# Performance work log

Hardware: AMD Instinct MI355X
Metric: run time of the kernel (lower is better)

The kernel has to match this reference:

```python
import jax, jax.numpy as jnp
import numpy as np

N_NODES = 100000

def setup_inputs() -> dict:
    key = jax.random.key(0)
    k1, k2, k3, k4, k5 = jax.random.split(key, 5)
    n_edges = 3200000
    row = jax.random.randint(k1, (n_edges,), 0, N_NODES)
    col = jax.random.randint(k2, (n_edges,), 0, N_NODES)
    vals = jax.random.uniform(k3, (n_edges,), dtype=jnp.float32)
    x = jax.random.normal(k4, (N_NODES, 128), dtype=jnp.float32)
    weight = jax.random.normal(k5, (128, 128), dtype=jnp.float32) * 0.05
    return {"row": row, "col": col, "vals": vals, "x": x, "weight": weight}

def reference(row, col, vals, x, weight):
    # SpMM: z[r] += vals[e] * x[col[e]]  (COO aggregation, equiv. to spmm_gpu over all blocks)
    gathered = vals[:, None] * x[col]                       # [E, F] gather + scale
    z = jax.ops.segment_sum(gathered, row, num_segments=N_NODES)  # [N, F] scatter-add
    return z @ weight                                        # dense GEMM [N, F] x [F, O]
```

## Files before the change

### kernel.cpp

```cpp
#include <hip/hip_runtime.h>
#include <hip/hip_bf16.h>

#define FDIM 128
#define BROWS 256
#define NBMAX 512
#define BCAP 9216
#define LDA 136

typedef __attribute__((ext_vector_type(8))) short short8v;
typedef __attribute__((ext_vector_type(4))) float f32x4;
typedef __attribute__((ext_vector_type(4))) unsigned uint4v;

__device__ __forceinline__ short f2bf(float f) {
    unsigned u = __float_as_uint(f);
    u += 0x7FFFu + ((u >> 16) & 1u);
    return (short)(u >> 16);
}

__global__ __launch_bounds__(256)
void gemm_mfma(const float* __restrict__ x, const float* __restrict__ W,
               unsigned short* __restrict__ y, int nrows) {
    __shared__ short ldsA[32 * LDA];
    const int lane = threadIdx.x & 63;
    const int wid  = threadIdx.x >> 6;
    const int colHalf = wid & 1;
    const int rowSub  = wid >> 1;
    const int l15 = lane & 15;
    const int lhi = lane >> 4;

    short8v bfrag[4][4];
    #pragma unroll
    for (int ks = 0; ks < 4; ++ks)
      #pragma unroll
      for (int ct = 0; ct < 4; ++ct) {
        const int col = colHalf * 64 + ct * 16 + l15;
        const int kb  = ks * 32 + lhi * 8;
        short8v f;
        #pragma unroll
        for (int j = 0; j < 8; ++j) f[j] = f2bf(W[(kb + j) * FDIM + col]);
        bfrag[ks][ct] = f;
      }

    const int lr  = threadIdx.x >> 3;
    const int lc  = (threadIdx.x & 7) * 16;

    const int nTiles = (nrows + 31) >> 5;
    for (int tile = blockIdx.x; tile < nTiles; tile += gridDim.x) {
        const int rowBase = tile * 32 + rowSub * 16;
        {
            int srow = tile * 32 + lr;
            if (srow >= nrows) srow = nrows - 1;
            const float* xp = x + (size_t)srow * FDIM + lc;
            float4 a = *(const float4*)(xp + 0);
            float4 b = *(const float4*)(xp + 4);
            float4 c = *(const float4*)(xp + 8);
            float4 d = *(const float4*)(xp + 12);
            short8v s0, s1;
            s0[0]=f2bf(a.x); s0[1]=f2bf(a.y); s0[2]=f2bf(a.z); s0[3]=f2bf(a.w);
            s0[4]=f2bf(b.x); s0[5]=f2bf(b.y); s0[6]=f2bf(b.z); s0[7]=f2bf(b.w);
            s1[0]=f2bf(c.x); s1[1]=f2bf(c.y); s1[2]=f2bf(c.z); s1[3]=f2bf(c.w);
            s1[4]=f2bf(d.x); s1[5]=f2bf(d.y); s1[6]=f2bf(d.z); s1[7]=f2bf(d.w);
            *(short8v*)&ldsA[lr * LDA + lc]     = s0;
            *(short8v*)&ldsA[lr * LDA + lc + 8] = s1;
        }
        __syncthreads();

        f32x4 acc[4] = {};
        #pragma unroll
        for (int ks = 0; ks < 4; ++ks) {
            short8v af = *(const short8v*)&ldsA[(rowSub * 16 + l15) * LDA + ks * 32 + lhi * 8];
            #pragma unroll
            for (int ct = 0; ct < 4; ++ct)
                acc[ct] = __builtin_amdgcn_mfma_f32_16x16x32_bf16(af, bfrag[ks][ct], acc[ct], 0, 0, 0);
        }
        #pragma unroll
        for (int ct = 0; ct < 4; ++ct) {
            const int col = colHalf * 64 + ct * 16 + l15;
            #pragma unroll
            for (int r = 0; r < 4; ++r) {
                int orow = rowBase + lhi * 4 + r;
                if (orow < nrows) y[(size_t)orow * FDIM + col] = (unsigned short)f2bf(acc[ct][r]);
            }
        }
        __syncthreads();
    }
}

__global__ __launch_bounds__(256)
void scatter_alloc(const int* __restrict__ row, const int* __restrict__ col,
                   const float* __restrict__ vals, int* __restrict__ gcur,
                   int2* __restrict__ skv1, int E, int per, int NB) {
    __shared__ int lc[NBMAX];
    __shared__ int cur[NBMAX];
    const int blk = blockIdx.x;
    for (int i = threadIdx.x; i < NB; i += 256) lc[i] = 0;
    __syncthreads();
    const int lo = blk * per;
    const int hi = (lo + per < E) ? lo + per : E;
    for (int i = lo + threadIdx.x; i < hi; i += 256)
        atomicAdd(&lc[row[i] >> 8], 1);
    __syncthreads();
    for (int i = threadIdx.x; i < NB; i += 256) {
        int c = lc[i];
        int base = c ? atomicAdd(&gcur[i], c) : 0;
        cur[i] = i * BCAP + base;
    }
    __syncthreads();
    for (int i = lo + threadIdx.x; i < hi; i += 256) {
        int r = row[i];
        int b = r >> 8;
        int pos = atomicAdd(&cur[b], 1);
        if (pos < (b + 1) * BCAP)
            skv1[pos] = make_int2(col[i] | ((r & 255) << 17), __float_as_int(vals[i]));
    }
}

__global__ __launch_bounds__(1024)
void sort_inplace(int2* __restrict__ skv1, const int* __restrict__ gcur,
                  int2* __restrict__ offs, int NB, int N) {
    __shared__ int2 ekv[BCAP];
    __shared__ int cnt[BROWS];
    __shared__ int cur[BROWS];
    __shared__ int ws4[4];
    const int tid = threadIdx.x;
    const int b   = blockIdx.x;
    const int start = b * BCAP;
    int total = gcur[b];
    if (total > BCAP) total = BCAP;

    if (tid < BROWS) cnt[tid] = 0;
    __syncthreads();
    for (int j = tid; j < total; j += 1024) {
        int2 kv = skv1[start + j];
        ekv[j] = kv;
        atomicAdd(&cnt[((unsigned)kv.x >> 17) & 255], 1);
    }
    __syncthreads();

    int c = 0, s = 0;
    if (tid < BROWS) {
        c = cnt[tid];
        s = c;
        const int lane = tid & 63;
        #pragma unroll
        for (int off = 1; off < 64; off <<= 1) {
            int t = __shfl_up(s, off, 64);
            if (lane >= off) s += t;
        }
        if (lane == 63) ws4[tid >> 6] = s;
    }
    __syncthreads();
    if (tid == 0) {
        int a0 = ws4[0], a1 = ws4[1], a2 = ws4[2];
        ws4[0] = 0; ws4[1] = a0; ws4[2] = a0 + a1; ws4[3] = a0 + a1 + a2;
    }
    __syncthreads();
    if (tid < BROWS) {
        int excl = s - c + ws4[tid >> 6];
        cur[tid] = excl;
        int gr = b * BROWS + tid;
        if (gr < N) offs[gr] = make_int2(start + excl, start + excl + c);
    }
    __syncthreads();

    for (int j = tid; j < total; j += 1024) {
        int2 kv = ekv[j];
        int rl = ((unsigned)kv.x >> 17) & 255;
        int pos = atomicAdd(&cur[rl], 1);
        skv1[start + pos] = make_int2(kv.x & 0x1FFFF, kv.y);
    }
}

__global__ __launch_bounds__(256)
void spmm_csr_v3(const int2* __restrict__ offs, const int2* __restrict__ skv,
                 const unsigned* __restrict__ yu, float* __restrict__ out, int N) {
    const int wid  = (blockIdx.x * 256 + threadIdx.x) >> 6;
    const int lane = threadIdx.x & 63;
    if (wid >= N) return;
    const int l15 = lane & 15;
    const int grp = lane >> 4;
    const int2 st = offs[wid];
    const int s = st.x, t = st.y;

    float accA[8] = {0,0,0,0,0,0,0,0};
    float accB[8] = {0,0,0,0,0,0,0,0};

    int e = s;
    for (; e + 8 <= t; e += 8) {
        int2 kA = skv[e + grp];
        int2 kB = skv[e + 4 + grp];
        uint4v uA = *(const uint4v*)&yu[(size_t)kA.x * 64 + l15 * 4];
        uint4v uB = *(const uint4v*)&yu[(size_t)kB.x * 64 + l15 * 4];
        float vA = __int_as_float(kA.y);
        float vB = __int_as_float(kB.y);
        #pragma unroll
        for (int j = 0; j < 4; ++j) {
            accA[2*j]   = fmaf(vA, __uint_as_float(uA[j] << 16),          accA[2*j]);
            accA[2*j+1] = fmaf(vA, __uint_as_float(uA[j] & 0xffff0000u), accA[2*j+1]);
            accB[2*j]   = fmaf(vB, __uint_as_float(uB[j] << 16),          accB[2*j]);
            accB[2*j+1] = fmaf(vB, __uint_as_float(uB[j] & 0xffff0000u), accB[2*j+1]);
        }
    }
    for (; e < t; e += 4) {
        int eA = e + grp;
        bool ok = eA < t;
        int2 kA = ok ? skv[eA] : make_int2(0, 0);
        uint4v uA = *(const uint4v*)&yu[(size_t)kA.x * 64 + l15 * 4];
        float vA = ok ? __int_as_float(kA.y) : 0.f;
        #pragma unroll
        for (int j = 0; j < 4; ++j) {
            accA[2*j]   = fmaf(vA, __uint_as_float(uA[j] << 16),          accA[2*j]);
            accA[2*j+1] = fmaf(vA, __uint_as_float(uA[j] & 0xffff0000u), accA[2*j+1]);
        }
    }
    #pragma unroll
    for (int j = 0; j < 8; ++j) {
        float a = accA[j] + accB[j];
        a += __shfl_xor(a, 16, 64);
        a += __shfl_xor(a, 32, 64);
        accA[j] = a;
    }
    if (grp == 0) {
        float* po = out + (size_t)wid * FDIM + l15 * 8;
        *(float4*)po       = make_float4(accA[0], accA[1], accA[2], accA[3]);
        *(float4*)(po + 4) = make_float4(accA[4], accA[5], accA[6], accA[7]);
    }
}

__global__ __launch_bounds__(256)
void edge_histogram(const int* __restrict__ row, int* __restrict__ counts, int E) {
    int i = blockIdx.x * 256 + threadIdx.x;
    if (i < E) atomicAdd(&counts[row[i]], 1);
}

__global__ __launch_bounds__(1024)
void scan_counts_v3(const int* __restrict__ counts, int* __restrict__ offsets,
                    int* __restrict__ cursor, int n, int ncopies, int stride) {
    const int tid  = threadIdx.x;
    const int lane = tid & 63;
    const int wv   = tid >> 6;
    __shared__ int waveSum[16];
    int carry = 0;
    const int nTiles = (n + 4095) >> 12;
    for (int tile = 0; tile < nTiles; ++tile) {
        const int idx = tile * 4096 + tid * 4;
        int4 v = make_int4(0, 0, 0, 0);
        if (idx + 3 < n) {
            for (int k = 0; k < ncopies; ++k) {
                int4 t = *(const int4*)&counts[(size_t)k * stride + idx];
                v.x += t.x; v.y += t.y; v.z += t.z; v.w += t.w;
            }
        } else if (idx < n) {
            for (int k = 0; k < ncopies; ++k) {
                const int* c = counts + (size_t)k * stride;
                v.x += c[idx];
                if (idx + 1 < n) v.y += c[idx + 1];
                if (idx + 2 < n) v.z += c[idx + 2];
            }
        }
        int s4 = v.x + v.y + v.z + v.w;
        int s = s4;
        #pragma unroll
        for (int off = 1; off < 64; off <<= 1) {
            int t = __shfl_up(s, off, 64);
            if (lane >= off) s += t;
        }
        if (lane == 63) waveSum[wv] = s;
        __syncthreads();
        if (tid < 64) {
            int ws = (tid < 16) ? waveSum[tid] : 0;
            #pragma unroll
            for (int off = 1; off < 16; off <<= 1) {
                int t = __shfl_up(ws, off, 64);
                if (lane >= off) ws += t;
            }
            if (tid < 16) waveSum[tid] = ws;
        }
        __syncthreads();
        const int waveBase = (wv == 0) ? 0 : waveSum[wv - 1];
        const int tileTot  = waveSum[15];
        int incl = s + waveBase + carry;
        int e0 = incl - s4;
        int4 o = make_int4(e0, e0 + v.x, e0 + v.x + v.y, e0 + v.x + v.y + v.z);
        if (idx + 3 < n) {
            *(int4*)&offsets[idx] = o;
            *(int4*)&cursor[idx]  = o;
        } else if (idx < n) {
            offsets[idx] = o.x;  cursor[idx] = o.x;
            if (idx + 1 < n) { offsets[idx + 1] = o.y; cursor[idx + 1] = o.y; }
            if (idx + 2 < n) { offsets[idx + 2] = o.z; cursor[idx + 2] = o.z; }
        }
        carry += tileTot;
        __syncthreads();
    }
    if (tid == 0) offsets[n] = carry;
}

__global__ __launch_bounds__(256)
void edge_scatter_chunked(const int* __restrict__ row, const int* __restrict__ col,
                          const float* __restrict__ vals, int* __restrict__ cursor,
                          int2* __restrict__ skv, int E, int rowsPerChunk) {
    const int chunk = blockIdx.x & 7;
    const int sub   = blockIdx.x >> 3;
    const int nsub  = gridDim.x >> 3;
    const int lo = chunk * rowsPerChunk;
    const int hi = lo + rowsPerChunk;
    for (int i = sub * 256 + threadIdx.x; i < E; i += nsub * 256) {
        int r = row[i];
        if (r >= lo && r < hi) {
            int pos = atomicAdd(&cursor[r], 1);
            skv[pos] = make_int2(col[i], __float_as_int(vals[i]));
        }
    }
}

__global__ __launch_bounds__(256)
void spmm_csr_v2(const int* __restrict__ offsets, const int2* __restrict__ skv,
                 const unsigned* __restrict__ yu, float* __restrict__ out, int N) {
    const int wid  = (blockIdx.x * 256 + threadIdx.x) >> 6;
    const int lane = threadIdx.x & 63;
    if (wid >= N) return;
    const int l15 = lane & 15;
    const int grp = lane >> 4;
    const int s = offsets[wid], t = offsets[wid + 1];

    float accA[8] = {0,0,0,0,0,0,0,0};
    float accB[8] = {0,0,0,0,0,0,0,0};

    int e = s;
    for (; e + 8 <= t; e += 8) {
        int2 kA = skv[e + grp];
        int2 kB = skv[e + 4 + grp];
        uint4v uA = *(const uint4v*)&yu[(size_t)kA.x * 64 + l15 * 4];
        uint4v uB = *(const uint4v*)&yu[(size_t)kB.x * 64 + l15 * 4];
        float vA = __int_as_float(kA.y);
        float vB = __int_as_float(kB.y);
        #pragma unroll
        for (int j = 0; j < 4; ++j) {
            accA[2*j]   = fmaf(vA, __uint_as_float(uA[j] << 16),          accA[2*j]);
            accA[2*j+1] = fmaf(vA, __uint_as_float(uA[j] & 0xffff0000u), accA[2*j+1]);
            accB[2*j]   = fmaf(vB, __uint_as_float(uB[j] << 16),          accB[2*j]);
            accB[2*j+1] = fmaf(vB, __uint_as_float(uB[j] & 0xffff0000u), accB[2*j+1]);
        }
    }
    for (; e < t; e += 4) {
        int eA = e + grp;
        bool ok = eA < t;
        int2 kA = ok ? skv[eA] : make_int2(0, 0);
        uint4v uA = *(const uint4v*)&yu[(size_t)kA.x * 64 + l15 * 4];
        float vA = ok ? __int_as_float(kA.y) : 0.f;
        #pragma unroll
        for (int j = 0; j < 4; ++j) {
            accA[2*j]   = fmaf(vA, __uint_as_float(uA[j] << 16),          accA[2*j]);
            accA[2*j+1] = fmaf(vA, __uint_as_float(uA[j] & 0xffff0000u), accA[2*j+1]);
        }
    }
    #pragma unroll
    for (int j = 0; j < 8; ++j) {
        float a = accA[j] + accB[j];
        a += __shfl_xor(a, 16, 64);
        a += __shfl_xor(a, 32, 64);
        accA[j] = a;
    }
    if (grp == 0) {
        float* po = out + (size_t)wid * FDIM + l15 * 8;
        *(float4*)po       = make_float4(accA[0], accA[1], accA[2], accA[3]);
        *(float4*)(po + 4) = make_float4(accA[4], accA[5], accA[6], accA[7]);
    }
}

__global__ __launch_bounds__(256)
void gemm_rows(const float* src, const float* __restrict__ W, float* dst, int nrows) {
    __shared__ float sW[FDIM * FDIM];
    for (int i = threadIdx.x; i < FDIM * FDIM; i += 256) sW[i] = W[i];
    __syncthreads();
    const int lane = threadIdx.x & 63;
    const int wid  = (blockIdx.x * 256 + threadIdx.x) >> 6;
    const int nw   = (gridDim.x * 256) >> 6;
    for (int n = wid; n < nrows; n += nw) {
        const float* xr = src + (size_t)n * FDIM;
        float acc0 = 0.f, acc1 = 0.f;
        #pragma unroll 8
        for (int k = 0; k < FDIM; ++k) {
            float xv = xr[k];
            float2 w = *(const float2*)&sW[k * FDIM + lane * 2];
            acc0 = fmaf(xv, w.x, acc0);
            acc1 = fmaf(xv, w.y, acc1);
        }
        *(float2*)&dst[(size_t)n * FDIM + lane * 2] = make_float2(acc0, acc1);
    }
}

__global__ __launch_bounds__(256)
void spmm_scatter(const int* __restrict__ row, const int* __restrict__ col,
                  const float* __restrict__ vals, const float* __restrict__ y,
                  float* __restrict__ out, int E) {
    long long tid = (long long)blockIdx.x * 256 + threadIdx.x;
    int e = (int)(tid >> 5);
    if (e >= E) return;
    int c = ((int)tid & 31) << 2;
    int r  = row[e];
    int cl = col[e];
    float v = vals[e];
    float4 yv = *(const float4*)&y[(size_t)cl * FDIM + c];
    float* po = out + (size_t)r * FDIM + c;
    unsafeAtomicAdd(po + 0, v * yv.x);
    unsafeAtomicAdd(po + 1, v * yv.y);
    unsafeAtomicAdd(po + 2, v * yv.z);
    unsafeAtomicAdd(po + 3, v * yv.w);
}

extern "C" void kernel_launch(void* const* d_in, const int* in_sizes, int n_in,
                              void* d_out, int out_size, void* d_ws, size_t ws_size,
                              hipStream_t stream) {
    const int*   row  = (const int*)d_in[0];
    const int*   col  = (const int*)d_in[1];
    const float* vals = (const float*)d_in[2];
    const float* x    = (const float*)d_in[3];
    const float* W    = (const float*)d_in[4];
    float* out = (float*)d_out;

    const int E = in_sizes[0];
    const int N = in_sizes[3] / FDIM;
    const int NB = (N + BROWS - 1) / BROWS;

    char* p = (char*)d_ws;
    unsigned short* yb = (unsigned short*)p;  p += (size_t)N * FDIM * 2;
    int*  gcur = (int*)p;   p += ((size_t)NB * 4 + 15) & ~(size_t)15;
    int2* offs = (int2*)p;  p += (size_t)N * 8;
    int2* skv1 = (int2*)p;  p += (size_t)NB * BCAP * 8;
    const size_t needA = (size_t)(p - (char*)d_ws);

    char* q = (char*)d_ws;
    unsigned short* ybB = (unsigned short*)q;  q += (size_t)N * FDIM * 2;
    int*  countsB  = (int*)q;  q += (size_t)N * 4;
    int*  offsetsB = (int*)q;  q += (size_t)(N + 1) * 4 + 12;
    int*  cursorB  = (int*)q;  q += (size_t)N * 4;
    int2* skvB     = (int2*)q; q += (size_t)E * 8;
    const size_t needB = (size_t)(q - (char*)d_ws);

    const int eb = (E + 255) / 256;
    const int rowsPerChunk = (N + 7) / 8;

    if (ws_size >= needA && NB <= NBMAX) {
        const int Bs = 512;
        const int per = (E + Bs - 1) / Bs;
        hipMemsetAsync(gcur, 0, (size_t)NB * 4, stream);
        gemm_mfma<<<512, 256, 0, stream>>>(x, W, yb, N);
        scatter_alloc<<<Bs, 256, 0, stream>>>(row, col, vals, gcur, skv1, E, per, NB);
        sort_inplace<<<NB, 1024, 0, stream>>>(skv1, gcur, offs, NB, N);
        spmm_csr_v3<<<((size_t)N * 64 + 255) / 256, 256, 0, stream>>>(offs, skv1, (const unsigned*)yb, out, N);
    } else if (ws_size >= needB) {
        hipMemsetAsync(countsB, 0, (size_t)N * 4, stream);
        gemm_mfma<<<512, 256, 0, stream>>>(x, W, ybB, N);
        edge_histogram<<<eb, 256, 0, stream>>>(row, countsB, E);
        scan_counts_v3<<<1, 1024, 0, stream>>>(countsB, offsetsB, cursorB, N, 1, 0);
        edge_scatter_chunked<<<2048, 256, 0, stream>>>(row, col, vals, cursorB, skvB, E, rowsPerChunk);
        spmm_csr_v2<<<((size_t)N * 64 + 255) / 256, 256, 0, stream>>>(offsetsB, skvB, (const unsigned*)ybB, out, N);
    } else if (ws_size >= (size_t)N * FDIM * 4) {
        float* yw = (float*)d_ws;
        hipMemsetAsync(d_out, 0, (size_t)out_size * sizeof(float), stream);
        gemm_rows<<<1024, 256, 0, stream>>>(x, W, yw, N);
        spmm_scatter<<<(E + 7) / 8, 256, 0, stream>>>(row, col, vals, yw, out, E);
    } else {
        hipMemsetAsync(d_out, 0, (size_t)out_size * sizeof(float), stream);
        spmm_scatter<<<(E + 7) / 8, 256, 0, stream>>>(row, col, vals, x, out, E);
        gemm_rows<<<1024, 256, 0, stream>>>(out, W, out, N);
    }
}
```

Baseline: 201.0 us.

## Fuse bucket sort into SpMM kernel using LDS-resident sorted edge indices

Merges the in-place bucket sort and the CSR SpMM into one kernel. Each block sorts its bucket's edges in LDS through an index permutation and then aggregates its rows straight from LDS, so the sorted edges are never written back to global memory and re-read, and one kernel launch plus the offsets array go away. Buckets shrink from 256 to 128 rows with a smaller capacity so the LDS footprint (edges plus indices) stays bounded, which doubles the block count. The trade-off is fewer, heavier blocks with one row per wave at a time, which may give less latency hiding for the gathers than the separate SpMM kernel, and the smaller per-bucket capacity gives less headroom against overflow.

```diff
diff --git a/kernel.cpp b/kernel.cpp
--- a/kernel.cpp
+++ b/kernel.cpp
@@ -2,9 +2,9 @@
 #include <hip/hip_bf16.h>
 
 #define FDIM 128
-#define BROWS 256
-#define NBMAX 512
-#define BCAP 9216
+#define BROWS 128
+#define BCAP 4800
+#define NBMX 1024
 #define LDA 136
 
 typedef __attribute__((ext_vector_type(8))) short short8v;
@@ -90,15 +90,15 @@
 void scatter_alloc(const int* __restrict__ row, const int* __restrict__ col,
                    const float* __restrict__ vals, int* __restrict__ gcur,
                    int2* __restrict__ skv1, int E, int per, int NB) {
-    __shared__ int lc[NBMAX];
-    __shared__ int cur[NBMAX];
+    __shared__ int lc[NBMX];
+    __shared__ int cur[NBMX];
     const int blk = blockIdx.x;
     for (int i = threadIdx.x; i < NB; i += 256) lc[i] = 0;
     __syncthreads();
     const int lo = blk * per;
     const int hi = (lo + per < E) ? lo + per : E;
     for (int i = lo + threadIdx.x; i < hi; i += 256)
-        atomicAdd(&lc[row[i] >> 8], 1);
+        atomicAdd(&lc[row[i] >> 7], 1);
     __syncthreads();
     for (int i = threadIdx.x; i < NB; i += 256) {
         int c = lc[i];
@@ -108,32 +108,35 @@
     __syncthreads();
     for (int i = lo + threadIdx.x; i < hi; i += 256) {
         int r = row[i];
-        int b = r >> 8;
+        int b = r >> 7;
         int pos = atomicAdd(&cur[b], 1);
         if (pos < (b + 1) * BCAP)
-            skv1[pos] = make_int2(col[i] | ((r & 255) << 17), __float_as_int(vals[i]));
-    }
-}
-
-__global__ __launch_bounds__(1024)
-void sort_inplace(int2* __restrict__ skv1, const int* __restrict__ gcur,
-                  int2* __restrict__ offs, int NB, int N) {
+            skv1[pos] = make_int2(col[i] | ((r & 127) << 17), __float_as_int(vals[i]));
+    }
+}
+
+__global__ __launch_bounds__(512)
+void sort_spmm(const int2* __restrict__ skv1, const int* __restrict__ gcur,
+               const unsigned* __restrict__ yu, float* __restrict__ out,
+               int NB, int N) {
     __shared__ int2 ekv[BCAP];
+    __shared__ unsigned short sidx[BCAP];
     __shared__ int cnt[BROWS];
+    __shared__ int rstart[BROWS];
     __shared__ int cur[BROWS];
-    __shared__ int ws4[4];
+    __shared__ int ws2[2];
     const int tid = threadIdx.x;
     const int b   = blockIdx.x;
-    const int start = b * BCAP;
+    const int gbase = b * BCAP;
     int total = gcur[b];
     if (total > BCAP) total = BCAP;
 
     if (tid < BROWS) cnt[tid] = 0;
     __syncthreads();
-    for (int j = tid; j < total; j += 1024) {
-        int2 kv = skv1[start + j];
+    for (int j = tid; j < total; j += 512) {
+        int2 kv = skv1[gbase + j];
         ekv[j] = kv;
-        atomicAdd(&cnt[((unsigned)kv.x >> 17) & 255], 1);
+        atomicAdd(&cnt[((unsigned)kv.x >> 17) & 127], 1);
     }
     __syncthreads();
 
@@ -147,83 +150,74 @@
             int t = __shfl_up(s, off, 64);
             if (lane >= off) s += t;
         }
-        if (lane == 63) ws4[tid >> 6] = s;
-    }
-    __syncthreads();
-    if (tid == 0) {
-        int a0 = ws4[0], a1 = ws4[1], a2 = ws4[2];
-        ws4[0] = 0; ws4[1] = a0; ws4[2] = a0 + a1; ws4[3] = a0 + a1 + a2;
-    }
+        if (lane == 63) ws2[tid >> 6] = s;
+    }
+    __syncthreads();
+    if (tid == 0) { int a0 = ws2[0]; ws2[0] = 0; ws2[1] = a0; }
     __syncthreads();
     if (tid < BROWS) {
-        int excl = s - c + ws4[tid >> 6];
-        cur[tid] = excl;
-        int gr = b * BROWS + tid;
-        if (gr < N) offs[gr] = make_int2(start + excl, start + excl + c);
-    }
-    __syncthreads();
-
-    for (int j = tid; j < total; j += 1024) {
-        int2 kv = ekv[j];
-        int rl = ((unsigned)kv.x >> 17) & 255;
+        int excl = s - c + ws2[tid >> 6];
+        rstart[tid] = excl;
+        cur[tid]    = excl;
+    }
+    __syncthreads();
+    for (int j = tid; j < total; j += 512) {
+        int rl = ((unsigned)ekv[j].x >> 17) & 127;
         int pos = atomicAdd(&cur[rl], 1);
-        skv1[start + pos] = make_int2(kv.x & 0x1FFFF, kv.y);
-    }
-}
-
-__global__ __launch_bounds__(256)
-void spmm_csr_v3(const int2* __restrict__ offs, const int2* __restrict__ skv,
-                 const unsigned* __restrict__ yu, float* __restrict__ out, int N) {
-    const int wid  = (blockIdx.x * 256 + threadIdx.x) >> 6;
-    const int lane = threadIdx.x & 63;
-    if (wid >= N) return;
-    const int l15 = lane & 15;
-    const int grp = lane >> 4;
-    const int2 st = offs[wid];
-    const int s = st.x, t = st.y;
-
-    float accA[8] = {0,0,0,0,0,0,0,0};
-    float accB[8] = {0,0,0,0,0,0,0,0};
-
-    int e = s;
-    for (; e + 8 <= t; e += 8) {
-        int2 kA = skv[e + grp];
-        int2 kB = skv[e + 4 + grp];
-        uint4v uA = *(const uint4v*)&yu[(size_t)kA.x * 64 + l15 * 4];
-        uint4v uB = *(const uint4v*)&yu[(size_t)kB.x * 64 + l15 * 4];
-        float vA = __int_as_float(kA.y);
-        float vB = __int_as_float(kB.y);
-        #pragma unroll
-        for (int j = 0; j < 4; ++j) {
-            accA[2*j]   = fmaf(vA, __uint_as_float(uA[j] << 16),          accA[2*j]);
-            accA[2*j+1] = fmaf(vA, __uint_as_float(uA[j] & 0xffff0000u), accA[2*j+1]);
-            accB[2*j]   = fmaf(vB, __uint_as_float(uB[j] << 16),          accB[2*j]);
-            accB[2*j+1] = fmaf(vB, __uint_as_float(uB[j] & 0xffff0000u), accB[2*j+1]);
-        }
-    }
-    for (; e < t; e += 4) {
-        int eA = e + grp;
-        bool ok = eA < t;
-        int2 kA = ok ? skv[eA] : make_int2(0, 0);
-        uint4v uA = *(const uint4v*)&yu[(size_t)kA.x * 64 + l15 * 4];
-        float vA = ok ? __int_as_float(kA.y) : 0.f;
-        #pragma unroll
-        for (int j = 0; j < 4; ++j) {
-            accA[2*j]   = fmaf(vA, __uint_as_float(uA[j] << 16),          accA[2*j]);
-            accA[2*j+1] = fmaf(vA, __uint_as_float(uA[j] & 0xffff0000u), accA[2*j+1]);
-        }
-    }
-    #pragma unroll
-    for (int j = 0; j < 8; ++j) {
-        float a = accA[j] + accB[j];
-        a += __shfl_xor(a, 16, 64);
-        a += __shfl_xor(a, 32, 64);
-        accA[j] = a;
-    }
-    if (grp == 0) {
-        float* po = out + (size_t)wid * FDIM + l15 * 8;
-        *(float4*)po       = make_float4(accA[0], accA[1], accA[2], accA[3]);
-        *(float4*)(po + 4) = make_float4(accA[4], accA[5], accA[6], accA[7]);
+        sidx[pos] = (unsigned short)j;
+    }
+    __syncthreads();
+
+    const int lane = tid & 63;
+    const int wv   = tid >> 6;
+    const int l15  = lane & 15;
+    const int grp  = lane >> 4;
+    for (int rr = wv; rr < BROWS; rr += 8) {
+        const int s0 = rstart[rr];
+        const int t0 = s0 + cnt[rr];
+        float accA[8] = {0,0,0,0,0,0,0,0};
+        float accB[8] = {0,0,0,0,0,0,0,0};
+        int e = s0;
+        for (; e + 8 <= t0; e += 8) {
+            int2 kA = ekv[sidx[e + grp]];
+            int2 kB = ekv[sidx[e + 4 + grp]];
+            uint4v uA = *(const uint4v*)&yu[(size_t)((unsigned)kA.x & 0x1FFFFu) * 64 + l15 * 4];
+            uint4v uB = *(const uint4v*)&yu[(size_t)((unsigned)kB.x & 0x1FFFFu) * 64 + l15 * 4];
+            float vA = __int_as_float(kA.y);
+            float vB = __int_as_float(kB.y);
+            #pragma unroll
+            for (int j = 0; j < 4; ++j) {
+                accA[2*j]   = fmaf(vA, __uint_as_float(uA[j] << 16),          accA[2*j]);
+                accA[2*j+1] = fmaf(vA, __uint_as_float(uA[j] & 0xffff0000u), accA[2*j+1]);
+                accB[2*j]   = fmaf(vB, __uint_as_float(uB[j] << 16),          accB[2*j]);
+                accB[2*j+1] = fmaf(vB, __uint_as_float(uB[j] & 0xffff0000u), accB[2*j+1]);
+            }
+        }
+        for (; e < t0; e += 4) {
+            int eA = e + grp;
+            bool ok = eA < t0;
+            int2 kA = ekv[sidx[ok ? eA : e]];
+            uint4v uA = *(const uint4v*)&yu[(size_t)((unsigned)kA.x & 0x1FFFFu) * 64 + l15 * 4];
+            float vA = ok ? __int_as_float(kA.y) : 0.f;
+            #pragma unroll
+            for (int j = 0; j < 4; ++j) {
+                accA[2*j]   = fmaf(vA, __uint_as_float(uA[j] << 16),          accA[2*j]);
+                accA[2*j+1] = fmaf(vA, __uint_as_float(uA[j] & 0xffff0000u), accA[2*j+1]);
+            }
+        }
+        #pragma unroll
+        for (int j = 0; j < 8; ++j) {
+            float a = accA[j] + accB[j];
+            a += __shfl_xor(a, 16, 64);
+            a += __shfl_xor(a, 32, 64);
+            accA[j] = a;
+        }
+        const int orow = b * BROWS + rr;
+        if (grp == 0 && orow < N) {
+            float* po = out + (size_t)orow * FDIM + l15 * 8;
+            *(float4*)po       = make_float4(accA[0], accA[1], accA[2], accA[3]);
+            *(float4*)(po + 4) = make_float4(accA[4], accA[5], accA[6], accA[7]);
+        }
     }
 }
 
@@ -427,7 +421,6 @@
     char* p = (char*)d_ws;
     unsigned short* yb = (unsigned short*)p;  p += (size_t)N * FDIM * 2;
     int*  gcur = (int*)p;   p += ((size_t)NB * 4 + 15) & ~(size_t)15;
-    int2* offs = (int2*)p;  p += (size_t)N * 8;
     int2* skv1 = (int2*)p;  p += (size_t)NB * BCAP * 8;
     const size_t needA = (size_t)(p - (char*)d_ws);
 
@@ -442,14 +435,13 @@
     const int eb = (E + 255) / 256;
     const int rowsPerChunk = (N + 7) / 8;
 
-    if (ws_size >= needA && NB <= NBMAX) {
+    if (ws_size >= needA && NB <= NBMX) {
         const int Bs = 512;
         const int per = (E + Bs - 1) / Bs;
         hipMemsetAsync(gcur, 0, (size_t)NB * 4, stream);
         gemm_mfma<<<512, 256, 0, stream>>>(x, W, yb, N);
         scatter_alloc<<<Bs, 256, 0, stream>>>(row, col, vals, gcur, skv1, E, per, NB);
-        sort_inplace<<<NB, 1024, 0, stream>>>(skv1, gcur, offs, NB, N);
-        spmm_csr_v3<<<((size_t)N * 64 + 255) / 256, 256, 0, stream>>>(offs, skv1, (const unsigned*)yb, out, N);
+        sort_spmm<<<NB, 512, 0, stream>>>(skv1, gcur, (const unsigned*)yb, out, NB, N);
     } else if (ws_size >= needB) {
         hipMemsetAsync(countsB, 0, (size_t)N * 4, stream);
         gemm_mfma<<<512, 256, 0, stream>>>(x, W, ybB, N);
```

Result: slower. 222.3 us (+10.6%).

## Co-schedule GEMM and edge scatter in one launch; unroll SpMM to four edge streams

Applied to the files above, without the earlier changes.

Merges the bf16 MFMA GEMM and the bucketed edge scatter into a single kernel whose blocks are split by block index. The two independent stages can then run concurrently on the GPU, and one launch boundary goes away. The SpMM kernel now keeps four independent accumulators and processes 16 edges per iteration, giving more gathers in flight to hide memory latency. The cost is higher register pressure in the SpMM and mixed LDS and register needs in the fused kernel, which may lower occupancy.

```diff
diff --git a/kernel.cpp b/kernel.cpp
--- a/kernel.cpp
+++ b/kernel.cpp
@@ -18,8 +18,239 @@
 }
 
 __global__ __launch_bounds__(256)
-void gemm_mfma(const float* __restrict__ x, const float* __restrict__ W,
-               unsigned short* __restrict__ y, int nrows) {
+void gemm_scatter(const float* __restrict__ x, const float* __restrict__ W,
+                  unsigned short* __restrict__ y, int nrows,
+                  const int* __restrict__ row, const int* __restrict__ col,
+                  const float* __restrict__ vals, int* __restrict__ gcur,
+                  int2* __restrict__ skv1, int E, int per, int NB, int GB) {
+    if ((int)blockIdx.x < GB) {
+        __shared__ short ldsA[32 * LDA];
+        const int lane = threadIdx.x & 63;
+        const int wid  = threadIdx.x >> 6;
+        const int colHalf = wid & 1;
+        const int rowSub  = wid >> 1;
+        const int l15 = lane & 15;
+        const int lhi = lane >> 4;
+
+        short8v bfrag[4][4];
+        #pragma unroll
+        for (int ks = 0; ks < 4; ++ks)
+          #pragma unroll
+          for (int ct = 0; ct < 4; ++ct) {
+            const int c = colHalf * 64 + ct * 16 + l15;
+            const int kb = ks * 32 + lhi * 8;
+            short8v f;
+            #pragma unroll
+            for (int j = 0; j < 8; ++j) f[j] = f2bf(W[(kb + j) * FDIM + c]);
+            bfrag[ks][ct] = f;
+          }
+
+        const int lr = threadIdx.x >> 3;
+        const int lc = (threadIdx.x & 7) * 16;
+
+        const int nTiles = (nrows + 31) >> 5;
+        for (int tile = blockIdx.x; tile < nTiles; tile += GB) {
+            const int rowBase = tile * 32 + rowSub * 16;
+            {
+                int srow = tile * 32 + lr;
+                if (srow >= nrows) srow = nrows - 1;
+                const float* xp = x + (size_t)srow * FDIM + lc;
+                float4 a = *(const float4*)(xp + 0);
+                float4 b = *(const float4*)(xp + 4);
+                float4 c = *(const float4*)(xp + 8);
+                float4 d = *(const float4*)(xp + 12);
+                short8v s0, s1;
+                s0[0]=f2bf(a.x); s0[1]=f2bf(a.y); s0[2]=f2bf(a.z); s0[3]=f2bf(a.w);
+                s0[4]=f2bf(b.x); s0[5]=f2bf(b.y); s0[6]=f2bf(b.z); s0[7]=f2bf(b.w);
+                s1[0]=f2bf(c.x); s1[1]=f2bf(c.y); s1[2]=f2bf(c.z); s1[3]=f2bf(c.w);
+                s1[4]=f2bf(d.x); s1[5]=f2bf(d.y); s1[6]=f2bf(d.z); s1[7]=f2bf(d.w);
+                *(short8v*)&ldsA[lr * LDA + lc]     = s0;
+                *(short8v*)&ldsA[lr * LDA + lc + 8] = s1;
+            }
+            __syncthreads();
+
+            f32x4 acc[4] = {};
+            #pragma unroll
+            for (int ks = 0; ks < 4; ++ks) {
+                short8v af = *(const short8v*)&ldsA[(rowSub * 16 + l15) * LDA + ks * 32 + lhi * 8];
+                #pragma unroll
+                for (int ct = 0; ct < 4; ++ct)
+                    acc[ct] = __builtin_amdgcn_mfma_f32_16x16x32_bf16(af, bfrag[ks][ct], acc[ct], 0, 0, 0);
+            }
+            #pragma unroll
+            for (int ct = 0; ct < 4; ++ct) {
+                const int c = colHalf * 64 + ct * 16 + l15;
+                #pragma unroll
+                for (int r = 0; r < 4; ++r) {
+                    int orow = rowBase + lhi * 4 + r;
+                    if (orow < nrows) y[(size_t)orow * FDIM + c] = (unsigned short)f2bf(acc[ct][r]);
+                }
+            }
+            __syncthreads();
+        }
+    } else {
+        __shared__ int lc[NBMAX];
+        __shared__ int cur[NBMAX];
+        const int blk = (int)blockIdx.x - GB;
+        for (int i = threadIdx.x; i < NB; i += 256) lc[i] = 0;
+        __syncthreads();
+        const int lo = blk * per;
+        const int hi = (lo + per < E) ? lo + per : E;
+        for (int i = lo + threadIdx.x; i < hi; i += 256)
+            atomicAdd(&lc[row[i] >> 8], 1);
+        __syncthreads();
+        for (int i = threadIdx.x; i < NB; i += 256) {
+            int c = lc[i];
+            int base = c ? atomicAdd(&gcur[i], c) : 0;
+            cur[i] = i * BCAP + base;
+        }
+        __syncthreads();
+        for (int i = lo + threadIdx.x; i < hi; i += 256) {
+            int r = row[i];
+            int b = r >> 8;
+            int pos = atomicAdd(&cur[b], 1);
+            if (pos < (b + 1) * BCAP)
+                skv1[pos] = make_int2(col[i] | ((r & 255) << 17), __float_as_int(vals[i]));
+        }
+    }
+}
+
+__global__ __launch_bounds__(1024)
+void sort_inplace(int2* __restrict__ skv1, const int* __restrict__ gcur,
+                  int2* __restrict__ offs, int NB, int N) {
+    __shared__ int2 ekv[BCAP];
+    __shared__ int cnt[BROWS];
+    __shared__ int cur[BROWS];
+    __shared__ int ws4[4];
+    const int tid = threadIdx.x;
+    const int b   = blockIdx.x;
+    const int start = b * BCAP;
+    int total = gcur[b];
+    if (total > BCAP) total = BCAP;
+
+    if (tid < BROWS) cnt[tid] = 0;
+    __syncthreads();
+    for (int j = tid; j < total; j += 1024) {
+        int2 kv = skv1[start + j];
+        ekv[j] = kv;
+        atomicAdd(&cnt[((unsigned)kv.x >> 17) & 255], 1);
+    }
+    __syncthreads();
+
+    int c = 0, s = 0;
+    if (tid < BROWS) {
+        c = cnt[tid];
+        s = c;
+        const int lane = tid & 63;
+        #pragma unroll
+        for (int off = 1; off < 64; off <<= 1) {
+            int t = __shfl_up(s, off, 64);
+            if (lane >= off) s += t;
+        }
+        if (lane == 63) ws4[tid >> 6] = s;
+    }
+    __syncthreads();
+    if (tid == 0) {
+        int a0 = ws4[0], a1 = ws4[1], a2 = ws4[2];
+        ws4[0] = 0; ws4[1] = a0; ws4[2] = a0 + a1; ws4[3] = a0 + a1 + a2;
+    }
+    __syncthreads();
+    if (tid < BROWS) {
+        int excl = s - c + ws4[tid >> 6];
+        cur[tid] = excl;
+        int gr = b * BROWS + tid;
+        if (gr < N) offs[gr] = make_int2(start + excl, start + excl + c);
+    }
+    __syncthreads();
+
+    for (int j = tid; j < total; j += 1024) {
+        int2 kv = ekv[j];
+        int rl = ((unsigned)kv.x >> 17) & 255;
+        int pos = atomicAdd(&cur[rl], 1);
+        skv1[start + pos] = make_int2(kv.x & 0x1FFFF, kv.y);
+    }
+}
+
+__global__ __launch_bounds__(256)
+void spmm_csr_v4(const int2* __restrict__ offs, const int2* __restrict__ skv,
+                 const unsigned* __restrict__ yu, float* __restrict__ out, int N) {
+    const int wid  = (blockIdx.x * 256 + threadIdx.x) >> 6;
+    const int lane = threadIdx.x & 63;
+    if (wid >= N) return;
+    const int l15 = lane & 15;
+    const int grp = lane >> 4;
+    const int2 st = offs[wid];
+    const int s = st.x, t = st.y;
+
+    float acc[4][8] = {};
+
+    int e = s;
+    for (; e + 16 <= t; e += 16) {
+        int2 k0 = skv[e + grp];
+        int2 k1 = skv[e + 4 + grp];
+        int2 k2 = skv[e + 8 + grp];
+        int2 k3 = skv[e + 12 + grp];
+        uint4v u0 = *(const uint4v*)&yu[(size_t)k0.x * 64 + l15 * 4];
+        uint4v u1 = *(const uint4v*)&yu[(size_t)k1.x * 64 + l15 * 4];
+        uint4v u2 = *(const uint4v*)&yu[(size_t)k2.x * 64 + l15 * 4];
+        uint4v u3 = *(const uint4v*)&yu[(size_t)k3.x * 64 + l15 * 4];
+        float v0 = __int_as_float(k0.y), v1 = __int_as_float(k1.y);
+        float v2 = __int_as_float(k2.y), v3 = __int_as_float(k3.y);
+        #pragma unroll
+        for (int j = 0; j < 4; ++j) {
+            acc[0][2*j]   = fmaf(v0, __uint_as_float(u0[j] << 16),          acc[0][2*j]);
+            acc[0][2*j+1] = fmaf(v0, __uint_as_float(u0[j] & 0xffff0000u), acc[0][2*j+1]);
+            acc[1][2*j]   = fmaf(v1, __uint_as_float(u1[j] << 16),          acc[1][2*j]);
+            acc[1][2*j+1] = fmaf(v1, __uint_as_float(u1[j] & 0xffff0000u), acc[1][2*j+1]);
+            acc[2][2*j]   = fmaf(v2, __uint_as_float(u2[j] << 16),          acc[2][2*j]);
+            acc[2][2*j+1] = fmaf(v2, __uint_as_float(u2[j] & 0xffff0000u), acc[2][2*j+1]);
+            acc[3][2*j]   = fmaf(v3, __uint_as_float(u3[j] << 16),          acc[3][2*j]);
+            acc[3][2*j+1] = fmaf(v3, __uint_as_float(u3[j] & 0xffff0000u), acc[3][2*j+1]);
+        }
+    }
+    for (; e + 8 <= t; e += 8) {
+        int2 k0 = skv[e + grp];
+        int2 k1 = skv[e + 4 + grp];
+        uint4v u0 = *(const uint4v*)&yu[(size_t)k0.x * 64 + l15 * 4];
+        uint4v u1 = *(const uint4v*)&yu[(size_t)k1.x * 64 + l15 * 4];
+        float v0 = __int_as_float(k0.y), v1 = __int_as_float(k1.y);
+        #pragma unroll
+        for (int j = 0; j < 4; ++j) {
+            acc[0][2*j]   = fmaf(v0, __uint_as_float(u0[j] << 16),          acc[0][2*j]);
+            acc[0][2*j+1] = fmaf(v0, __uint_as_float(u0[j] & 0xffff0000u), acc[0][2*j+1]);
+            acc[1][2*j]   = fmaf(v1, __uint_as_float(u1[j] << 16),          acc[1][2*j]);
+            acc[1][2*j+1] = fmaf(v1, __uint_as_float(u1[j] & 0xffff0000u), acc[1][2*j+1]);
+        }
+    }
+    for (; e < t; e += 4) {
+        int eA = e + grp;
+        bool ok = eA < t;
+        int2 k0 = ok ? skv[eA] : make_int2(0, 0);
+        uint4v u0 = *(const uint4v*)&yu[(size_t)k0.x * 64 + l15 * 4];
+        float v0 = ok ? __int_as_float(k0.y) : 0.f;
+        #pragma unroll
+        for (int j = 0; j < 4; ++j) {
+            acc[0][2*j]   = fmaf(v0, __uint_as_float(u0[j] << 16),          acc[0][2*j]);
+            acc[0][2*j+1] = fmaf(v0, __uint_as_float(u0[j] & 0xffff0000u), acc[0][2*j+1]);
+        }
+    }
+    #pragma unroll
+    for (int j = 0; j < 8; ++j) {
+        float a = (acc[0][j] + acc[1][j]) + (acc[2][j] + acc[3][j]);
+        a += __shfl_xor(a, 16, 64);
+        a += __shfl_xor(a, 32, 64);
+        acc[0][j] = a;
+    }
+    if (grp == 0) {
+        float* po = out + (size_t)wid * FDIM + l15 * 8;
+        *(float4*)po       = make_float4(acc[0][0], acc[0][1], acc[0][2], acc[0][3]);
+        *(float4*)(po + 4) = make_float4(acc[0][4], acc[0][5], acc[0][6], acc[0][7]);
+    }
+}
+
+__global__ __launch_bounds__(256)
+void gemm_mfma_only(const float* __restrict__ x, const float* __restrict__ W,
+                    unsigned short* __restrict__ y, int nrows) {
     __shared__ short ldsA[32 * LDA];
     const int lane = threadIdx.x & 63;
     const int wid  = threadIdx.x >> 6;
@@ -33,16 +264,16 @@
     for (int ks = 0; ks < 4; ++ks)
       #pragma unroll
       for (int ct = 0; ct < 4; ++ct) {
-        const int col = colHalf * 64 + ct * 16 + l15;
-        const int kb  = ks * 32 + lhi * 8;
+        const int c = colHalf * 64 + ct * 16 + l15;
+        const int kb = ks * 32 + lhi * 8;
         short8v f;
         #pragma unroll
-        for (int j = 0; j < 8; ++j) f[j] = f2bf(W[(kb + j) * FDIM + col]);
+        for (int j = 0; j < 8; ++j) f[j] = f2bf(W[(kb + j) * FDIM + c]);
         bfrag[ks][ct] = f;
       }
 
-    const int lr  = threadIdx.x >> 3;
-    const int lc  = (threadIdx.x & 7) * 16;
+    const int lr = threadIdx.x >> 3;
+    const int lc = (threadIdx.x & 7) * 16;
 
     const int nTiles = (nrows + 31) >> 5;
     for (int tile = blockIdx.x; tile < nTiles; tile += gridDim.x) {
@@ -75,155 +306,14 @@
         }
         #pragma unroll
         for (int ct = 0; ct < 4; ++ct) {
-            const int col = colHalf * 64 + ct * 16 + l15;
+            const int c = colHalf * 64 + ct * 16 + l15;
             #pragma unroll
             for (int r = 0; r < 4; ++r) {
                 int orow = rowBase + lhi * 4 + r;
-                if (orow < nrows) y[(size_t)orow * FDIM + col] = (unsigned short)f2bf(acc[ct][r]);
-            }
-        }
-        __syncthreads();
-    }
-}
-
-__global__ __launch_bounds__(256)
-void scatter_alloc(const int* __restrict__ row, const int* __restrict__ col,
-                   const float* __restrict__ vals, int* __restrict__ gcur,
-                   int2* __restrict__ skv1, int E, int per, int NB) {
-    __shared__ int lc[NBMAX];
-    __shared__ int cur[NBMAX];
-    const int blk = blockIdx.x;
-    for (int i = threadIdx.x; i < NB; i += 256) lc[i] = 0;
-    __syncthreads();
-    const int lo = blk * per;
-    const int hi = (lo + per < E) ? lo + per : E;
-    for (int i = lo + threadIdx.x; i < hi; i += 256)
-        atomicAdd(&lc[row[i] >> 8], 1);
-    __syncthreads();
-    for (int i = threadIdx.x; i < NB; i += 256) {
-        int c = lc[i];
-        int base = c ? atomicAdd(&gcur[i], c) : 0;
-        cur[i] = i * BCAP + base;
-    }
-    __syncthreads();
-    for (int i = lo + threadIdx.x; i < hi; i += 256) {
-        int r = row[i];
-        int b = r >> 8;
-        int pos = atomicAdd(&cur[b], 1);
-        if (pos < (b + 1) * BCAP)
-            skv1[pos] = make_int2(col[i] | ((r & 255) << 17), __float_as_int(vals[i]));
-    }
-}
-
-__global__ __launch_bounds__(1024)
-void sort_inplace(int2* __restrict__ skv1, const int* __restrict__ gcur,
-                  int2* __restrict__ offs, int NB, int N) {
-    __shared__ int2 ekv[BCAP];
-    __shared__ int cnt[BROWS];
-    __shared__ int cur[BROWS];
-    __shared__ int ws4[4];
-    const int tid = threadIdx.x;
-    const int b   = blockIdx.x;
-    const int start = b * BCAP;
-    int total = gcur[b];
-    if (total > BCAP) total = BCAP;
-
-    if (tid < BROWS) cnt[tid] = 0;
-    __syncthreads();
-    for (int j = tid; j < total; j += 1024) {
-        int2 kv = skv1[start + j];
-        ekv[j] = kv;
-        atomicAdd(&cnt[((unsigned)kv.x >> 17) & 255], 1);
-    }
-    __syncthreads();
-
-    int c = 0, s = 0;
-    if (tid < BROWS) {
-        c = cnt[tid];
-        s = c;
-        const int lane = tid & 63;
-        #pragma unroll
-        for (int off = 1; off < 64; off <<= 1) {
-            int t = __shfl_up(s, off, 64);
-            if (lane >= off) s += t;
-        }
-        if (lane == 63) ws4[tid >> 6] = s;
-    }
-    __syncthreads();
-    if (tid == 0) {
-        int a0 = ws4[0], a1 = ws4[1], a2 = ws4[2];
-        ws4[0] = 0; ws4[1] = a0; ws4[2] = a0 + a1; ws4[3] = a0 + a1 + a2;
-    }
-    __syncthreads();
-    if (tid < BROWS) {
-        int excl = s - c + ws4[tid >> 6];
-        cur[tid] = excl;
-        int gr = b * BROWS + tid;
-        if (gr < N) offs[gr] = make_int2(start + excl, start + excl + c);
-    }
-    __syncthreads();
-
-    for (int j = tid; j < total; j += 1024) {
-        int2 kv = ekv[j];
-        int rl = ((unsigned)kv.x >> 17) & 255;
-        int pos = atomicAdd(&cur[rl], 1);
-        skv1[start + pos] = make_int2(kv.x & 0x1FFFF, kv.y);
-    }
-}
-
-__global__ __launch_bounds__(256)
-void spmm_csr_v3(const int2* __restrict__ offs, const int2* __restrict__ skv,
-                 const unsigned* __restrict__ yu, float* __restrict__ out, int N) {
-    const int wid  = (blockIdx.x * 256 + threadIdx.x) >> 6;
-    const int lane = threadIdx.x & 63;
-    if (wid >= N) return;
-    const int l15 = lane & 15;
-    const int grp = lane >> 4;
-    const int2 st = offs[wid];
-    const int s = st.x, t = st.y;
-
-    float accA[8] = {0,0,0,0,0,0,0,0};
-    float accB[8] = {0,0,0,0,0,0,0,0};
-
-    int e = s;
-    for (; e + 8 <= t; e += 8) {
-        int2 kA = skv[e + grp];
-        int2 kB = skv[e + 4 + grp];
-        uint4v uA = *(const uint4v*)&yu[(size_t)kA.x * 64 + l15 * 4];
-        uint4v uB = *(const uint4v*)&yu[(size_t)kB.x * 64 + l15 * 4];
-        float vA = __int_as_float(kA.y);
-        float vB = __int_as_float(kB.y);
-        #pragma unroll
-        for (int j = 0; j < 4; ++j) {
-            accA[2*j]   = fmaf(vA, __uint_as_float(uA[j] << 16),          accA[2*j]);
-            accA[2*j+1] = fmaf(vA, __uint_as_float(uA[j] & 0xffff0000u), accA[2*j+1]);
-            accB[2*j]   = fmaf(vB, __uint_as_float(uB[j] << 16),          accB[2*j]);
-            accB[2*j+1] = fmaf(vB, __uint_as_float(uB[j] & 0xffff0000u), accB[2*j+1]);
-        }
-    }
-    for (; e < t; e += 4) {
-        int eA = e + grp;
-        bool ok = eA < t;
-        int2 kA = ok ? skv[eA] : make_int2(0, 0);
-        uint4v uA = *(const uint4v*)&yu[(size_t)kA.x * 64 + l15 * 4];
-        float vA = ok ? __int_as_float(kA.y) : 0.f;
-        #pragma unroll
-        for (int j = 0; j < 4; ++j) {
-            accA[2*j]   = fmaf(vA, __uint_as_float(uA[j] << 16),          accA[2*j]);
-            accA[2*j+1] = fmaf(vA, __uint_as_float(uA[j] & 0xffff0000u), accA[2*j+1]);
-        }
-    }
-    #pragma unroll
-    for (int j = 0; j < 8; ++j) {
-        float a = accA[j] + accB[j];
-        a += __shfl_xor(a, 16, 64);
-        a += __shfl_xor(a, 32, 64);
-        accA[j] = a;
-    }
-    if (grp == 0) {
-        float* po = out + (size_t)wid * FDIM + l15 * 8;
-        *(float4*)po       = make_float4(accA[0], accA[1], accA[2], accA[3]);
-        *(float4*)(po + 4) = make_float4(accA[4], accA[5], accA[6], accA[7]);
+                if (orow < nrows) y[(size_t)orow * FDIM + c] = (unsigned short)f2bf(acc[ct][r]);
+            }
+        }
+        __syncthreads();
     }
 }
 
@@ -443,16 +533,16 @@
     const int rowsPerChunk = (N + 7) / 8;
 
     if (ws_size >= needA && NB <= NBMAX) {
-        const int Bs = 512;
+        const int GB = 512, Bs = 512;
         const int per = (E + Bs - 1) / Bs;
         hipMemsetAsync(gcur, 0, (size_t)NB * 4, stream);
-        gemm_mfma<<<512, 256, 0, stream>>>(x, W, yb, N);
-        scatter_alloc<<<Bs, 256, 0, stream>>>(row, col, vals, gcur, skv1, E, per, NB);
+        gemm_scatter<<<GB + Bs, 256, 0, stream>>>(x, W, yb, N, row, col, vals,
+                                                  gcur, skv1, E, per, NB, GB);
         sort_inplace<<<NB, 1024, 0, stream>>>(skv1, gcur, offs, NB, N);
-        spmm_csr_v3<<<((size_t)N * 64 + 255) / 256, 256, 0, stream>>>(offs, skv1, (const unsigned*)yb, out, N);
+        spmm_csr_v4<<<((size_t)N * 64 + 255) / 256, 256, 0, stream>>>(offs, skv1, (const unsigned*)yb, out, N);
     } else if (ws_size >= needB) {
         hipMemsetAsync(countsB, 0, (size_t)N * 4, stream);
-        gemm_mfma<<<512, 256, 0, stream>>>(x, W, ybB, N);
+        gemm_mfma_only<<<512, 256, 0, stream>>>(x, W, ybB, N);
         edge_histogram<<<eb, 256, 0, stream>>>(row, countsB, E);
         scan_counts_v3<<<1, 1024, 0, stream>>>(countsB, offsetsB, cursorB, N, 1, 0);
         edge_scatter_chunked<<<2048, 256, 0, stream>>>(row, col, vals, cursorB, skvB, E, rowsPerChunk);
```

New measurement: 193.0 us. 1.04x faster.
